# Optimization experiments

Hardware: AMD Instinct MI355X
Metric: run time of the kernel (lower is better)

Reference implementation:

```python
import jax, jax.numpy as jnp
import numpy as np

N_ATOMS = 64
N_SAMPLES = 2 ** 15
SAMPLERATE = 22050
N_RES = 4096
N_ROOMS = 8
N_COEFFS = N_SAMPLES // 2 + 1


def make_waves():
    # musical_scale_hz(21, 106, 4096//4) -> 4 waveform families (sine, saw, square, triangle)
    n_steps = N_RES // 4
    midi = np.linspace(21.0, 106.0, n_steps)
    f0 = 440.0 * 2.0 ** ((midi - 69.0) / 12.0)
    rps = ((f0 / (SAMPLERATE / 2.0)) * np.pi).astype(np.float32)
    rad = rps[:, None] * np.arange(N_SAMPLES, dtype=np.float32)[None, :]
    sine = np.sin(rad)
    t = rad / (2.0 * np.pi)
    saw = (2.0 * (t - np.floor(t + 0.5))).astype(np.float32)
    sq = np.sign(sine).astype(np.float32)
    tri = (2.0 * np.abs(saw) - 1.0).astype(np.float32)
    return jnp.asarray(np.concatenate([sine, saw, sq, tri], 0).reshape(1, N_RES, N_SAMPLES))


def pdf2(means, stds, n):
    # gaussian pdf evaluated on linspace(0,1,n); means/stds: (1, A)
    rng = jnp.linspace(0.0, 1.0, n)
    mu = means[..., None]
    sd = stds[..., None]
    return jnp.exp(-0.5 * ((rng - mu) / sd) ** 2) / (sd * jnp.sqrt(2.0 * jnp.pi))


def linear_interp(x, n_out):
    # F.interpolate(mode='linear', align_corners=False) on last axis; x: (b, a, f)
    f = x.shape[-1]
    pos = (jnp.arange(n_out) + 0.5) * (f / n_out) - 0.5
    pos = jnp.clip(pos, 0.0, f - 1)
    i0 = jnp.floor(pos).astype(jnp.int32)
    i1 = jnp.minimum(i0 + 1, f - 1)
    w = (pos - i0).astype(x.dtype)
    return x[..., i0] * (1.0 - w) + x[..., i1] * w


def exponential_decay(decay_values, n_atoms, n_frames, base_resonance, n_samples):
    dv = jax.nn.sigmoid(decay_values.reshape(-1, n_atoms, 1))
    dv = jnp.broadcast_to(dv, (dv.shape[0], n_atoms, n_frames))
    decay = base_resonance + dv * (1.0 - base_resonance) * 0.95
    decay = jnp.exp(jnp.cumsum(jnp.log(decay + 1e-12), axis=-1))
    return linear_interp(decay, n_samples)


def fft_convolve(a, b):
    # zero-pad to 2N, multiply spectra, take first N samples
    n = a.shape[-1]
    pa = jnp.pad(a, ((0, 0), (0, 0), (0, n)))
    pb = jnp.pad(b, ((0, 0), (0, 0), (0, n)))
    spec = jnp.fft.rfft(pa, axis=-1) * jnp.fft.rfft(pb, axis=-1)
    return jnp.fft.irfft(spec, n=2 * n, axis=-1)[..., :n]


def layer_norm(x, w, b, eps=1e-5):
    m = jnp.mean(x, axis=-1, keepdims=True)
    v = jnp.var(x, axis=-1, keepdims=True)
    return (x - m) / jnp.sqrt(v + eps) * w + b


def sparse_softmax_st(x):
    soft = jax.nn.softmax(x, axis=-1)
    hard = jax.nn.one_hot(jnp.argmax(x, axis=-1), x.shape[-1], dtype=x.dtype)
    return hard + soft - jax.lax.stop_gradient(soft)


def model_forward(x, mix, decays, filter_decays, resonance_choice, noise_filter,
                  resonance_filter, resonance_filter2, env, amplitudes, verb_params,
                  noise, waves, ln_w, ln_b, mix_w1, mix_w2, room_w1, room_w2, room_irs):
    overall_mix = jax.nn.softmax(mix, axis=-1)                                   # (1,A,2)
    resonances = jnp.einsum('bar,brn->ban', jax.nn.relu(resonance_choice), waves)  # (1,A,N)

    # band-pass filtered noise (gaussian filter in frequency domain)
    noise_spec = jnp.fft.rfft(noise, axis=-1)
    noise_filt = pdf2(noise_filter[:, :, 0], jnp.abs(noise_filter[:, :, 1]) + 1e-12, N_COEFFS)
    filtered_noise = jnp.fft.irfft(noise_spec * noise_filt, n=N_SAMPLES, axis=-1)

    res_spec = jnp.fft.rfft(resonances, axis=-1)
    rf1 = pdf2(jnp.zeros_like(resonance_filter[:, :, 0]),
               jnp.abs(resonance_filter[:, :, 1]) + 1e-12, N_COEFFS)
    filtered_resonance = jnp.fft.irfft(res_spec * rf1, n=N_SAMPLES, axis=-1)
    rf2 = pdf2(jnp.zeros_like(resonance_filter2[:, :, 0]),
               jnp.abs(resonance_filter2[:, :, 1]) + 1e-12, N_COEFFS)
    filt_res_2 = jnp.fft.irfft(res_spec * rf2, n=N_SAMPLES, axis=-1)

    filt_crossfade = exponential_decay(filter_decays, N_ATOMS, 128, 0.02, N_SAMPLES)
    decay_env = exponential_decay(decays, N_ATOMS, 128, 0.02, N_SAMPLES)
    decaying_resonance = filtered_resonance * decay_env
    decaying_resonance2 = filt_res_2 * decay_env

    # gaussian envelope branch (gaussian_envelope = True)
    envelopes = pdf2(env[:, :, 0], jnp.abs(env[:, :, 1] + 1e-12) * 0.1, N_SAMPLES)
    positioned_noise = filtered_noise * envelopes

    res = fft_convolve(positioned_noise, decaying_resonance)
    res2 = fft_convolve(positioned_noise, decaying_resonance2)
    mixed = filt_crossfade * res + (1.0 - filt_crossfade) * res2

    final = positioned_noise * overall_mix[:, :, 0:1] + mixed * overall_mix[:, :, 1:2]
    final = final / (jnp.linalg.norm(final, axis=-1, keepdims=True) + 1e-8)
    amps = jnp.abs(amplitudes)
    final = final * amps

    # ReverbGenerator: layernorm -> small MLPs -> hard room choice -> fft convolve with IR
    h = layer_norm(verb_params, ln_w, ln_b)
    mix_v = jax.nn.sigmoid(jax.nn.leaky_relu(h @ mix_w1) @ mix_w2)               # (1,A,1)
    room_logits = jax.nn.leaky_relu(h @ room_w1) @ room_w2                        # (1,A,R)
    room = sparse_softmax_st(room_logits)
    ir = jnp.einsum('bar,rn->ban', room, room_irs)
    wet = fft_convolve(final, ir)
    out = final * mix_v + wet * (1.0 - mix_v)
    return out, amps


def setup_inputs() -> dict:
    key = jax.random.key(0)
    ks = jax.random.split(key, 20)
    return {
        'x': jax.random.normal(ks[0], (1, 1), jnp.float32),
        'mix': jax.random.uniform(ks[1], (1, N_ATOMS, 2), jnp.float32),
        'decays': jax.random.uniform(ks[2], (1, N_ATOMS, 1), jnp.float32, -6.0, 6.0),
        'filter_decays': jax.random.uniform(ks[3], (1, N_ATOMS, 1), jnp.float32, -6.0, 6.0),
        'resonance_choice': jax.random.uniform(ks[4], (1, N_ATOMS, N_RES), jnp.float32),
        'noise_filter': jax.random.uniform(ks[5], (1, N_ATOMS, 2), jnp.float32),
        'resonance_filter': jax.random.uniform(ks[6], (1, N_ATOMS, 2), jnp.float32),
        'resonance_filter2': jax.random.uniform(ks[7], (1, N_ATOMS, 2), jnp.float32),
        'env': jax.random.uniform(ks[8], (1, N_ATOMS, 2), jnp.float32),
        'amplitudes': jax.random.uniform(ks[9], (1, N_ATOMS, 1), jnp.float32) ** 2,
        'verb_params': jax.random.uniform(ks[10], (1, N_ATOMS, 4), jnp.float32, -1.0, 1.0),
        'noise': jax.random.uniform(ks[11], (1, N_ATOMS, N_SAMPLES), jnp.float32, -1.0, 1.0),
        'waves': make_waves(),
        'ln_w': jnp.ones((4,), jnp.float32),
        'ln_b': jnp.zeros((4,), jnp.float32),
        'mix_w1': jax.random.normal(ks[12], (4, 4), jnp.float32) * 0.1,
        'mix_w2': jax.random.normal(ks[13], (4, 1), jnp.float32) * 0.1,
        'room_w1': jax.random.normal(ks[14], (4, 4), jnp.float32) * 0.1,
        'room_w2': jax.random.normal(ks[15], (4, N_ROOMS), jnp.float32) * 0.1,
        'room_irs': jax.random.normal(ks[16], (N_ROOMS, N_SAMPLES), jnp.float32) * 0.01,
    }


def reference(x, mix, decays, filter_decays, resonance_choice, noise_filter,
              resonance_filter, resonance_filter2, env, amplitudes, verb_params,
              noise, waves, ln_w, ln_b, mix_w1, mix_w2, room_w1, room_w2, room_irs):
    return model_forward(x, mix, decays, filter_decays, resonance_choice, noise_filter,
                         resonance_filter, resonance_filter2, env, amplitudes, verb_params,
                         noise, waves, ln_w, ln_b, mix_w1, mix_w2, room_w1, room_w2, room_irs)
```

## Files before the change

### kernel.cpp

```cpp
#include <hip/hip_runtime.h>


typedef __attribute__((ext_vector_type(8))) short bf16x8;
typedef __attribute__((ext_vector_type(4))) float f32x4;

constexpr int SC_OM0   = 0;
constexpr int SC_OM1   = 64;
constexpr int SC_NFMU  = 128;
constexpr int SC_NFSD  = 192;
constexpr int SC_RF1SD = 256;
constexpr int SC_RF2SD = 320;
constexpr int SC_ENVMU = 384;
constexpr int SC_ENVSD = 448;
constexpr int SC_AMPS  = 512;
constexpr int SC_MIXV  = 576;
constexpr int SC_ROOM  = 832;
constexpr int SC_PSS   = 1024;
constexpr int SC_DTAB  = 4096;
constexpr int SC_FTAB  = 12288;

constexpr size_t OFF_SCAL = 0;
constexpr size_t OFF_CT   = 65536;
constexpr size_t OFF_P    = 327680;
constexpr size_t OFF_DS   = 8716288;
constexpr size_t OFF_RP   = OFF_DS;
constexpr size_t OFF_W64  = 17104896;
constexpr size_t OFF_NSS  = OFF_W64;
constexpr size_t OFF_W2   = OFF_W64 + 4194304;
constexpr size_t OFF_RSS  = 25493504;
constexpr size_t OFF_FINU = OFF_RSS;
constexpr size_t OFF_W1   = 29687808;
constexpr size_t OFF_FN   = 38076416;
constexpr size_t OFF_FR1  = 40173568;
constexpr size_t OFF_FR2  = 42270720;
constexpr size_t OFF_IRS  = 44367872;
constexpr size_t WS_FLOATS= 45416448;

__device__ __forceinline__ float2 cmul(float2 a, float2 b) {
  return make_float2(a.x*b.x - a.y*b.y, a.x*b.y + a.y*b.x);
}

__device__ __forceinline__ short f2bf(float x) {
  unsigned u = __float_as_uint(x);
  u = (u + 0x7FFFu + ((u >> 16) & 1u)) >> 16;
  return (short)u;
}

__device__ __forceinline__ void dft16(float2 d[16], float ei)
{
  const float CA[4] = {1.0f, 0.92387953251128674f, 0.70710678118654752f, 0.38268343236508977f};
  const float SA[4] = {0.0f, 0.38268343236508977f, 0.70710678118654752f, 0.92387953251128674f};
  const float CB[4] = {1.0f, 0.70710678118654752f, 0.0f, -0.70710678118654752f};
  const float SB[4] = {0.0f, 0.70710678118654752f, 1.0f, 0.70710678118654752f};
  float2 e[16];
  #pragma unroll
  for (int q = 0; q < 4; ++q) {
    float2 x0 = d[q], x1 = d[q+4], x2 = d[q+8], x3 = d[q+12];
    float ca = CA[q], sa = ei*SA[q], cb = CB[q], sb = ei*SB[q];
    float2 sum1 = make_float2(x0.x+x2.x, x0.y+x2.y);
    float2 d1   = make_float2(x0.x-x2.x, x0.y-x2.y);
    float2 dif1 = make_float2(d1.x*ca - d1.y*sa, d1.x*sa + d1.y*ca);
    float2 sum2 = make_float2(x1.x+x3.x, x1.y+x3.y);
    float2 d2   = make_float2(x1.x-x3.x, x1.y-x3.y);
    float2 dt   = make_float2(d2.x*ca - d2.y*sa, d2.x*sa + d2.y*ca);
    float2 dif2 = make_float2(-ei*dt.y, ei*dt.x);
    float2 Dm   = make_float2(sum1.x-sum2.x, sum1.y-sum2.y);
    float2 Dm2  = make_float2(dif1.x-dif2.x, dif1.y-dif2.y);
    e[4*q+0] = make_float2(sum1.x+sum2.x, sum1.y+sum2.y);
    e[4*q+1] = make_float2(dif1.x+dif2.x, dif1.y+dif2.y);
    e[4*q+2] = make_float2(Dm.x*cb - Dm.y*sb, Dm.x*sb + Dm.y*cb);
    e[4*q+3] = make_float2(Dm2.x*cb - Dm2.y*sb, Dm2.x*sb + Dm2.y*cb);
  }
  #pragma unroll
  for (int q = 0; q < 4; ++q) {
    float2 x0 = e[q], x1 = e[q+4], x2 = e[q+8], x3 = e[q+12];
    float2 sum1 = make_float2(x0.x+x2.x, x0.y+x2.y);
    float2 dif1 = make_float2(x0.x-x2.x, x0.y-x2.y);
    float2 sum2 = make_float2(x1.x+x3.x, x1.y+x3.y);
    float2 d2   = make_float2(x1.x-x3.x, x1.y-x3.y);
    float2 dif2 = make_float2(-ei*d2.y, ei*d2.x);
    d[q]    = make_float2(sum1.x+sum2.x, sum1.y+sum2.y);
    d[q+4]  = make_float2(dif1.x+dif2.x, dif1.y+dif2.y);
    d[q+8]  = make_float2(sum1.x-sum2.x, sum1.y-sum2.y);
    d[q+12] = make_float2(dif1.x-dif2.x, dif1.y-dif2.y);
  }
}

__device__ __forceinline__ void twiddleB(float2 d[16], int u, float dir2pi)
{
  float sn1, cs1;
  __sincosf(dir2pi * ((float)u * (1.0f/256.0f)), &sn1, &cs1);
  float2 w1 = make_float2(cs1, sn1);
  float2 tw = w1;
  #pragma unroll
  for (int k = 1; k < 16; ++k) { d[k] = cmul(d[k], tw); tw = cmul(tw, w1); }
}

template<int LEN>
__device__ float2* lds_fft(float2* src, float2* dst,
                           const float2* __restrict__ T256,
                           float dsign, float ei)
{
  constexpr int QB  = LEN >> 2;
  constexpr int FPT = (16 * QB) >> 8;
  constexpr int NST = (LEN == 256) ? 4 : 3;
  int n = LEN, s = 1, ls = 0;
  int sh = (LEN == 256) ? 0 : 1;

  if (LEN == 128) {
    constexpr int HB = LEN >> 1;
    constexpr int BPT = (16 * HB) >> 8;
    __syncthreads();
    #pragma unroll
    for (int b = 0; b < BPT; ++b) {
      int g = threadIdx.x + (b << 8);
      int row = g / HB;
      int beta = g & (HB - 1);
      float2 tj = T256[beta << 1];
      float cs = tj.x, sn = dsign * tj.y;
      float2 av = src[row*LEN + (beta ^ row)];
      float2 bv = src[row*LEN + ((beta + HB) ^ row)];
      float2 sum = make_float2(av.x + bv.x, av.y + bv.y);
      float2 dif = make_float2(av.x - bv.x, av.y - bv.y);
      float2 tw  = make_float2(dif.x*cs - dif.y*sn, dif.x*sn + dif.y*cs);
      dst[row*LEN + ((2*beta)     ^ row)] = sum;
      dst[row*LEN + ((2*beta + 1) ^ row)] = tw;
    }
    float2* t = src; src = dst; dst = t;
    n = 64; s = 2; ls = 1; sh = 2;
  }

  for (int st = 0; st < NST; ++st) {
    __syncthreads();
    #pragma unroll
    for (int b = 0; b < FPT; ++b) {
      int g   = threadIdx.x + (b << 8);
      int row = g / QB;
      int q   = g & (QB - 1);
      int p1  = q >> ls;
      int blo = q & (s - 1);
      int base = row * LEN;
      float2 x0 = src[base + ( q         ^ row)];
      float2 x1 = src[base + ((q +   QB) ^ row)];
      float2 x2 = src[base + ((q + 2*QB) ^ row)];
      float2 x3 = src[base + ((q + 3*QB) ^ row)];
      float2 tA = T256[p1 << sh];
      float caA = tA.x, saA = dsign * tA.y;
      float2 tB = T256[p1 << (sh + 1)];
      float caB = tB.x, saB = dsign * tB.y;
      float2 sum1 = make_float2(x0.x + x2.x, x0.y + x2.y);
      float2 d1   = make_float2(x0.x - x2.x, x0.y - x2.y);
      float2 dif1 = make_float2(d1.x*caA - d1.y*saA, d1.x*saA + d1.y*caA);
      float2 sum2 = make_float2(x1.x + x3.x, x1.y + x3.y);
      float2 d2   = make_float2(x1.x - x3.x, x1.y - x3.y);
      float2 dt   = make_float2(d2.x*caA - d2.y*saA, d2.x*saA + d2.y*caA);
      float2 dif2 = make_float2(-ei * dt.y, ei * dt.x);
      float2 S  = make_float2(sum1.x + sum2.x, sum1.y + sum2.y);
      float2 Dm = make_float2(sum1.x - sum2.x, sum1.y - sum2.y);
      float2 D  = make_float2(Dm.x*caB - Dm.y*saB, Dm.x*saB + Dm.y*caB);
      float2 S2 = make_float2(dif1.x + dif2.x, dif1.y + dif2.y);
      float2 Dm2= make_float2(dif1.x - dif2.x, dif1.y - dif2.y);
      float2 D2 = make_float2(Dm2.x*caB - Dm2.y*saB, Dm2.x*saB + Dm2.y*caB);
      int w0 = (p1 << (ls + 2)) | blo;
      dst[base + ( w0          ^ row)] = S;
      dst[base + ((w0 +     s) ^ row)] = S2;
      dst[base + ((w0 + 2 * s) ^ row)] = D;
      dst[base + ((w0 + 3 * s) ^ row)] = D2;
    }
    float2* t = src; src = dst; dst = t;
    n >>= 2; s <<= 2; ls += 2; sh += 2;
  }
  __syncthreads();
  return src;
}

template<int N1, int MODE_IN, int MODE_OUT>
__global__ __launch_bounds__(256) void k_fft_strided(
    float2* cbuf, const float* __restrict__ rin, const float* __restrict__ rin2,
    float* __restrict__ rout, float* __restrict__ rout2,
    const float* __restrict__ scal, const float* __restrict__ finU,
    float dir2pi, float outScale)
{
  constexpr int N  = N1 * 256;
  constexpr int NH = N >> 1;
  constexpr int LOG2N1 = (N1 == 256) ? 8 : 7;
  __shared__ float2 X[16*16*17];
  __shared__ float2 T256[256];
  __shared__ float2 TN[N1];
  const int a = blockIdx.y;
  const int n1base = blockIdx.x << 4;
  const int r = threadIdx.x & 15;
  const int u = threadIdx.x >> 4;
  const float ei = (dir2pi < 0.0f) ? -1.0f : 1.0f;

  {
    float ang = dir2pi * ((float)threadIdx.x * (1.0f/256.0f));
    float sn, cs; __sincosf(ang, &sn, &cs);
    T256[threadIdx.x] = make_float2(cs, sn);
    if (threadIdx.x < N1) {
      float ang2 = dir2pi * ((float)threadIdx.x * (1.0f/(float)N));
      float sn2, cs2; __sincosf(ang2, &sn2, &cs2);
      TN[threadIdx.x] = make_float2(cs2, sn2);
    }
  }

  float2 d[16];
  #pragma unroll
  for (int m = 0; m < 16; ++m) {
    int j = u + (m << 4);
    int n = n1base + r + N1 * j;
    float x = (n < NH) ? rin[(size_t)a * NH + n] : 0.0f;
    d[m] = make_float2(x, 0.0f);
  }

  dft16(d, ei);
  twiddleB(d, u, dir2pi);
  #pragma unroll
  for (int k = 0; k < 16; ++k) X[(u*16 + k)*17 + r] = d[k];
  __syncthreads();
  #pragma unroll
  for (int m = 0; m < 16; ++m) d[m] = X[(m*16 + u)*17 + r];
  dft16(d, ei);

  #pragma unroll
  for (int k1 = 0; k1 < 16; ++k1) {
    int j = u + (k1 << 4);
    int n = n1base + r + N1 * j;
    int aa = (n1base + r) * j;
    float2 tw = cmul(T256[(aa >> LOG2N1) & 255], TN[aa & (N1 - 1)]);
    cbuf[(size_t)a * N + n] = cmul(d[k1], tw);
  }
}

__global__ __launch_bounds__(256) void k_fft_s256_DsP(
    float2* __restrict__ Ds, float2* __restrict__ P,
    const float* __restrict__ fr1, const float* __restrict__ fr2,
    const float* __restrict__ fn, const float* __restrict__ scal)
{
  constexpr int N = 65536, NH = 32768;
  constexpr float FWD = -6.283185307179586f;
  __shared__ float2 X[16*16*17];
  __shared__ float2 T256[256];
  __shared__ float2 TN[256];
  const bool isDs = blockIdx.y < 64;
  const int a = isDs ? blockIdx.y : blockIdx.y - 64;
  const int n1base = blockIdx.x << 4;
  const int r = threadIdx.x & 15;
  const int u = threadIdx.x >> 4;

  {
    float ang = FWD * ((float)threadIdx.x * (1.0f/256.0f));
    float sn, cs; __sincosf(ang, &sn, &cs);
    T256[threadIdx.x] = make_float2(cs, sn);
    float ang2 = FWD * ((float)threadIdx.x * (1.0f/(float)N));
    float sn2, cs2; __sincosf(ang2, &sn2, &cs2);
    TN[threadIdx.x] = make_float2(cs2, sn2);
  }

  float emu = 0.f, esd = 1.f, egp = 0.f;
  if (!isDs) {
    emu = scal[SC_ENVMU + a];
    esd = scal[SC_ENVSD + a];
    egp = 0.3989422804014327f / esd;
  }

  float2 d[16];
  #pragma unroll
  for (int m = 0; m < 16; ++m) {
    int j = u + (m << 4);
    int n = n1base + r + 256 * j;
    float2 v = make_float2(0.0f, 0.0f);
    if (n < NH) {
      if (isDs) {
        float pos = ((float)n + 0.5f) * (1.0f/256.0f) - 0.5f;
        pos = fminf(fmaxf(pos, 0.0f), 127.0f);
        int i0 = (int)pos;
        float w = pos - (float)i0;
        int i1 = (i0 + 1 < 127) ? i0 + 1 : 127;
        const float* dt = scal + SC_DTAB + a*128;
        float de = dt[i0]*(1.0f-w) + dt[i1]*w;
        v = make_float2(fr1[(size_t)a * NH + n] * de,
                        fr2[(size_t)a * NH + n] * de);
      } else {
        float uu = (float)n * (1.0f / 32767.0f);
        float te = (uu - emu) / esd;
        float envv = __expf(-0.5f * te * te) * egp;
        v = make_float2(fn[(size_t)a * NH + n] * envv, 0.0f);
      }
    }
    d[m] = v;
  }

  dft16(d, -1.0f);
  twiddleB(d, u, FWD);
  #pragma unroll
  for (int k = 0; k < 16; ++k) X[(u*16 + k)*17 + r] = d[k];
  __syncthreads();
  #pragma unroll
  for (int m = 0; m < 16; ++m) d[m] = X[(m*16 + u)*17 + r];
  dft16(d, -1.0f);

  float2* outp = isDs ? Ds : P;
  #pragma unroll
  for (int k1 = 0; k1 < 16; ++k1) {
    int j = u + (k1 << 4);
    int n = n1base + r + 256 * j;
    int aa = (n1base + r) * j;
    float2 tw = cmul(T256[(aa >> 8) & 255], TN[aa & 255]);
    outp[(size_t)a * N + n] = cmul(d[k1], tw);
  }
}

__global__ __launch_bounds__(256) void k_fft_s128_first(
    float2* __restrict__ RSs, float2* __restrict__ NSs,
    const float* __restrict__ rez, const float* __restrict__ noise)
{
  constexpr int N1 = 128, N = 32768;
  constexpr float FWD = -6.283185307179586f;
  __shared__ float2 X[16*16*17];
  __shared__ float2 T256[256];
  __shared__ float2 TN[128];
  const bool isRS = blockIdx.y < 64;
  const int a = isRS ? blockIdx.y : blockIdx.y - 64;
  const int n1base = blockIdx.x << 4;
  const int r = threadIdx.x & 15;
  const int u = threadIdx.x >> 4;

  {
    float ang = FWD * ((float)threadIdx.x * (1.0f/256.0f));
    float sn, cs; __sincosf(ang, &sn, &cs);
    T256[threadIdx.x] = make_float2(cs, sn);
    if (threadIdx.x < 128) {
      float ang2 = FWD * ((float)threadIdx.x * (1.0f/(float)N));
      float sn2, cs2; __sincosf(ang2, &sn2, &cs2);
      TN[threadIdx.x] = make_float2(cs2, sn2);
    }
  }

  float2 d[16];
  #pragma unroll
  for (int m = 0; m < 16; ++m) {
    int j = u + (m << 4);
    int n = n1base + r + N1 * j;
    float x = isRS ? (rez[(size_t)a * N + n] + rez[(size_t)(64 + a) * N + n])
                   : noise[(size_t)a * N + n];
    d[m] = make_float2(x, 0.0f);
  }

  dft16(d, -1.0f);
  twiddleB(d, u, FWD);
  #pragma unroll
  for (int k = 0; k < 16; ++k) X[(u*16 + k)*17 + r] = d[k];
  __syncthreads();
  #pragma unroll
  for (int m = 0; m < 16; ++m) d[m] = X[(m*16 + u)*17 + r];
  dft16(d, -1.0f);

  float2* outp = isRS ? RSs : NSs;
  #pragma unroll
  for (int k1 = 0; k1 < 16; ++k1) {
    int j = u + (k1 << 4);
    int n = n1base + r + N1 * j;
    int aa = (n1base + r) * j;
    float2 tw = cmul(T256[(aa >> 7) & 255], TN[aa & 127]);
    outp[(size_t)a * N + n] = cmul(d[k1], tw);
  }
}

__global__ __launch_bounds__(256) void k_fft_m128_both(
    const float2* __restrict__ RSs, const float2* __restrict__ NSs,
    float2* __restrict__ W1, float2* __restrict__ W2,
    const float* __restrict__ scal)
{
  constexpr int N1 = 128;
  constexpr int N = N1 * 256;
  constexpr int ITERS = (16 * N1) >> 8;
  constexpr int LOG2N1 = 7;
  constexpr float FWD = -6.283185307179586f;
  constexpr float IVD = +6.283185307179586f;
  __shared__ float2 A[16 * N1];
  __shared__ float2 B[16 * N1];
  __shared__ float2 T256[256];
  __shared__ float2 TN[N1];
  const bool isRS = blockIdx.y < 64;
  const int a = isRS ? blockIdx.y : blockIdx.y - 64;
  const int colbase = blockIdx.x << 4;

  {
    float ang = FWD * ((float)threadIdx.x * (1.0f/256.0f));
    float sn, cs; __sincosf(ang, &sn, &cs);
    T256[threadIdx.x] = make_float2(cs, sn);
    if (threadIdx.x < N1) {
      float ang2 = IVD * ((float)threadIdx.x * (1.0f/(float)N));
      float sn2, cs2; __sincosf(ang2, &sn2, &cs2);
      TN[threadIdx.x] = make_float2(cs2, sn2);
    }
  }

  float mu = 0.f, isd1 = 0.f, g1 = 0.f, isd2 = 0.f, g2 = 0.f;
  if (isRS) {
    float s1 = scal[SC_RF1SD + a], s2 = scal[SC_RF2SD + a];
    isd1 = 1.0f/s1; g1 = 0.3989422804014327f/s1;
    isd2 = 1.0f/s2; g2 = 0.3989422804014327f/s2;
  } else {
    float sd = scal[SC_NFSD + a]; mu = scal[SC_NFMU + a];
    isd1 = 1.0f/sd; g1 = 0.3989422804014327f/sd;
  }
  const float2* zin = (isRS ? RSs : NSs) + (size_t)a * N;
  float2* out = (isRS ? W1 : W2) + (size_t)a * N;

  #pragma unroll
  for (int it = 0; it < ITERS; ++it) {
    int flat = threadIdx.x + (it << 8);
    int c = flat / N1, j = flat & (N1 - 1);
    A[c*N1 + (j ^ c)] = zin[(size_t)(colbase + c) * N1 + j];
  }
  float2* cur = lds_fft<N1>(A, B, T256, 1.0f, -1.0f);
  float2* alt = (cur == A) ? B : A;

  #pragma unroll
  for (int it = 0; it < ITERS; ++it) {
    int flat = threadIdx.x + (it << 8);
    int c = flat / N1, j = flat & (N1 - 1);
    int idx = c*N1 + (j ^ c);
    float2 v = cur[idx];
    int k  = (colbase + c) + (j << 8);
    int kk = (k <= N - k) ? k : N - k;
    if (isRS) {
      float fr = (float)kk * (2.0f/(float)N);
      float t1 = fr * isd1, t2 = fr * isd2;
      float ga = __expf(-0.5f * t1 * t1) * g1;
      float gb = __expf(-0.5f * t2 * t2) * g2;
      v = make_float2(v.x*ga - v.y*gb, v.x*gb + v.y*ga);
    } else {
      float t = ((float)kk * (2.0f/(float)N) - mu) * isd1;
      float g = __expf(-0.5f * t * t) * g1;
      v.x *= g; v.y *= g;
    }
    cur[idx] = v;
  }

  float2* r2 = lds_fft<N1>(cur, alt, T256, -1.0f, 1.0f);

  #pragma unroll
  for (int it = 0; it < ITERS; ++it) {
    int flat = threadIdx.x + (it << 8);
    int c = flat / N1, j = flat & (N1 - 1);
    float2 v = r2[c*N1 + (j ^ c)];
    int aa = j * (colbase + c);
    float2 t1 = T256[(aa >> LOG2N1) & 255];
    t1.y = -t1.y;
    float2 tw = cmul(t1, TN[aa & (N1 - 1)]);
    out[(size_t)(colbase + c) * N1 + j] = cmul(v, tw);
  }
}

__global__ __launch_bounds__(256) void k_fft_s128_last(
    const float2* __restrict__ W1, const float2* __restrict__ W2,
    float* __restrict__ fr1, float* __restrict__ fr2, float* __restrict__ fn)
{
  constexpr int N1 = 128, N = 32768;
  constexpr float IVD = +6.283185307179586f;
  constexpr float S32 = 1.0f / 32768.0f;
  __shared__ float2 X[16*16*17];
  const bool isRS = blockIdx.y < 64;
  const int a = isRS ? blockIdx.y : blockIdx.y - 64;
  const int n1base = blockIdx.x << 4;
  const int r = threadIdx.x & 15;
  const int u = threadIdx.x >> 4;

  const float2* cb = (isRS ? W1 : W2) + (size_t)a * N;
  float2 d[16];
  #pragma unroll
  for (int m = 0; m < 16; ++m) {
    int j = u + (m << 4);
    d[m] = cb[n1base + r + N1 * j];
  }
  dft16(d, 1.0f);
  twiddleB(d, u, IVD);
  #pragma unroll
  for (int k = 0; k < 16; ++k) X[(u*16 + k)*17 + r] = d[k];
  __syncthreads();
  #pragma unroll
  for (int m = 0; m < 16; ++m) d[m] = X[(m*16 + u)*17 + r];
  dft16(d, 1.0f);

  #pragma unroll
  for (int k1 = 0; k1 < 16; ++k1) {
    int j = u + (k1 << 4);
    int n = n1base + r + N1 * j;
    if (isRS) {
      fr1[(size_t)a * N + n] = d[k1].x * S32;
      fr2[(size_t)a * N + n] = d[k1].y * S32;
    } else {
      fn[(size_t)a * N + n] = d[k1].x * S32;
    }
  }
}

__global__ __launch_bounds__(256) void k_fft_mid256dual(
    const float2* __restrict__ zin, const float2* __restrict__ zin2half,
    float2* __restrict__ out1, const int* __restrict__ roomArr)
{
  constexpr int N = 65536;
  constexpr float FWD = -6.283185307179586f;
  constexpr float IVD = +6.283185307179586f;
  __shared__ float2 X[16*16*17];
  __shared__ float2 T256[256];
  __shared__ float2 TN[256];
  const int a = blockIdx.y;
  const int colbase = blockIdx.x << 4;
  const int u  = threadIdx.x & 15;
  const int rc = threadIdx.x >> 4;

  {
    float ang = FWD * ((float)threadIdx.x * (1.0f/256.0f));
    float sn, cs; __sincosf(ang, &sn, &cs);
    T256[threadIdx.x] = make_float2(cs, sn);
    float ang2 = IVD * ((float)threadIdx.x * (1.0f/(float)N));
    float sn2, cs2; __sincosf(ang2, &sn2, &cs2);
    TN[threadIdx.x] = make_float2(cs2, sn2);
  }
  __syncthreads();

  const float2* z2 = zin2half + (size_t)(roomArr ? roomArr[a] : a) * N;
  const size_t rowG = (size_t)a * N + (size_t)(colbase + rc) * 256;
  const size_t rowZ2 = (size_t)(colbase + rc) * 256;

  float2 d[16];
  #pragma unroll
  for (int m = 0; m < 16; ++m) d[m] = zin[rowG + u + (m << 4)];
  dft16(d, -1.0f);
  twiddleB(d, u, FWD);
  #pragma unroll
  for (int k = 0; k < 16; ++k) X[(rc*16 + k)*17 + u] = d[k];
  #pragma unroll
  for (int m = 0; m < 16; ++m) d[m] = X[(rc*16 + u)*17 + m];
  dft16(d, -1.0f);

  float2 stash[16];
  #pragma unroll
  for (int k = 0; k < 16; ++k) stash[k] = d[k];
  #pragma unroll
  for (int m = 0; m < 16; ++m) d[m] = z2[rowZ2 + u + (m << 4)];
  dft16(d, -1.0f);
  twiddleB(d, u, FWD);
  #pragma unroll
  for (int k = 0; k < 16; ++k) X[(rc*16 + k)*17 + u] = d[k];
  #pragma unroll
  for (int m = 0; m < 16; ++m) d[m] = X[(rc*16 + u)*17 + m];
  dft16(d, -1.0f);
  #pragma unroll
  for (int k = 0; k < 16; ++k) d[k] = cmul(stash[k], d[k]);

  dft16(d, 1.0f);
  twiddleB(d, u, IVD);
  #pragma unroll
  for (int k = 0; k < 16; ++k) X[(rc*16 + k)*17 + u] = d[k];
  #pragma unroll
  for (int m = 0; m < 16; ++m) d[m] = X[(rc*16 + u)*17 + m];
  dft16(d, 1.0f);

  #pragma unroll
  for (int k1 = 0; k1 < 16; ++k1) {
    int j = u + (k1 << 4);
    int aa = j * (colbase + rc);
    float2 t1 = T256[(aa >> 8) & 255];
    t1.y = -t1.y;
    float2 tw = cmul(t1, TN[aa & 255]);
    out1[rowG + j] = cmul(d[k1], tw);
  }
}

__global__ __launch_bounds__(256) void k_fft_out6fwd(
    const float2* __restrict__ W64in, const float* __restrict__ fn,
    float* __restrict__ finU, float* __restrict__ scal,
    float2* __restrict__ DsOut)
{
  constexpr int N = 65536, NH = 32768;
  constexpr float FWD = -6.283185307179586f;
  constexpr float IVD = +6.283185307179586f;
  constexpr float S64 = 1.0f / 65536.0f;
  __shared__ float2 X[16*16*17];
  __shared__ float2 T256[256];
  __shared__ float2 TN[256];
  __shared__ float red[256];
  const int a = blockIdx.y;
  const int n1base = blockIdx.x << 4;
  const int r = threadIdx.x & 15;
  const int u = threadIdx.x >> 4;

  {
    float ang = FWD * ((float)threadIdx.x * (1.0f/256.0f));
    float sn, cs; __sincosf(ang, &sn, &cs);
    T256[threadIdx.x] = make_float2(cs, sn);
    float ang2 = FWD * ((float)threadIdx.x * (1.0f/(float)N));
    float sn2, cs2; __sincosf(ang2, &sn2, &cs2);
    TN[threadIdx.x] = make_float2(cs2, sn2);
  }

  const float emu = scal[SC_ENVMU + a];
  const float esd = scal[SC_ENVSD + a];
  const float egp = 0.3989422804014327f / esd;
  const float om0 = scal[SC_OM0 + a], om1 = scal[SC_OM1 + a];
  const float* ft = scal + SC_FTAB + a*128;

  float2 d[16];
  #pragma unroll
  for (int m = 0; m < 16; ++m) {
    int j = u + (m << 4);
    d[m] = W64in[(size_t)a * N + n1base + r + 256 * j];
  }
  dft16(d, 1.0f);
  twiddleB(d, u, IVD);
  #pragma unroll
  for (int k = 0; k < 16; ++k) X[(u*16 + k)*17 + r] = d[k];
  __syncthreads();
  #pragma unroll
  for (int m = 0; m < 16; ++m) d[m] = X[(m*16 + u)*17 + r];
  dft16(d, 1.0f);

  float fv[8];
  float ss = 0.0f;
  #pragma unroll
  for (int k1 = 0; k1 < 8; ++k1) {
    int n = n1base + r + 256 * (u + (k1 << 4));
    float resv  = d[k1].x * S64;
    float res2v = d[k1].y * S64;
    float uu = (float)n * (1.0f / 32767.0f);
    float te = (uu - emu) / esd;
    float envv = __expf(-0.5f * te * te) * egp;
    float pnv = fn[(size_t)a * NH + n] * envv;
    float pos = ((float)n + 0.5f) * (1.0f/256.0f) - 0.5f;
    pos = fminf(fmaxf(pos, 0.0f), 127.0f);
    int i0 = (int)pos;
    float w = pos - (float)i0;
    int i1 = (i0 + 1 < 127) ? i0 + 1 : 127;
    float fc = ft[i0]*(1.0f-w) + ft[i1]*w;
    float f = pnv*om0 + (fc*resv + (1.0f-fc)*res2v)*om1;
    finU[(size_t)a * NH + n] = f;
    fv[k1] = f;
    ss += f * f;
  }
  red[threadIdx.x] = ss;
  __syncthreads();
  for (int s = 128; s > 0; s >>= 1) {
    if (threadIdx.x < s) red[threadIdx.x] += red[threadIdx.x + s];
    __syncthreads();
  }
  if (threadIdx.x == 0) scal[SC_PSS + a*16 + blockIdx.x] = red[0];

  #pragma unroll
  for (int m = 0; m < 16; ++m)
    d[m] = (m < 8) ? make_float2(fv[m], 0.0f) : make_float2(0.0f, 0.0f);
  dft16(d, -1.0f);
  twiddleB(d, u, FWD);
  #pragma unroll
  for (int k = 0; k < 16; ++k) X[(u*16 + k)*17 + r] = d[k];
  __syncthreads();
  #pragma unroll
  for (int m = 0; m < 16; ++m) d[m] = X[(m*16 + u)*17 + r];
  dft16(d, -1.0f);

  #pragma unroll
  for (int k1 = 0; k1 < 16; ++k1) {
    int j = u + (k1 << 4);
    int n = n1base + r + 256 * j;
    int aa = (n1base + r) * j;
    float2 tw = cmul(T256[(aa >> 8) & 255], TN[aa & 255]);
    DsOut[(size_t)a * N + n] = cmul(d[k1], tw);
  }
}

__global__ __launch_bounds__(256) void k_fft_s256_out3(
    const float2* __restrict__ W64in, const float* __restrict__ finU,
    const float* __restrict__ scal, float* __restrict__ out)
{
  constexpr int N = 65536, NH = 32768;
  constexpr float IVD = +6.283185307179586f;
  constexpr float S64 = 1.0f / 65536.0f;
  __shared__ float2 X[16*16*17];
  const int a = blockIdx.y;
  const int n1base = blockIdx.x << 4;
  const int r = threadIdx.x & 15;
  const int u = threadIdx.x >> 4;

  float ss = 0.0f;
  #pragma unroll
  for (int i = 0; i < 16; ++i) ss += scal[SC_PSS + a*16 + i];
  float fscale = scal[SC_AMPS + a] / (sqrtf(ss) + 1e-8f);
  float mixv = scal[SC_MIXV + a];
  float w1 = fscale * (1.0f - mixv);
  float w0 = fscale * mixv;

  float2 d[16];
  #pragma unroll
  for (int m = 0; m < 16; ++m) {
    int j = u + (m << 4);
    d[m] = W64in[(size_t)a * N + n1base + r + 256 * j];
  }
  dft16(d, 1.0f);
  twiddleB(d, u, IVD);
  #pragma unroll
  for (int k = 0; k < 16; ++k) X[(u*16 + k)*17 + r] = d[k];
  __syncthreads();
  #pragma unroll
  for (int m = 0; m < 16; ++m) d[m] = X[(m*16 + u)*17 + r];
  dft16(d, 1.0f);

  #pragma unroll
  for (int k1 = 0; k1 < 8; ++k1) {
    int n = n1base + r + 256 * (u + (k1 << 4));
    out[(size_t)a * NH + n] =
        d[k1].x * S64 * w1 + finU[(size_t)a * NH + n] * w0;
  }
}

__global__ void k_scalars(
    const float* __restrict__ mix, const float* __restrict__ decays,
    const float* __restrict__ fdec, const float* __restrict__ nf,
    const float* __restrict__ rf1, const float* __restrict__ rf2,
    const float* __restrict__ env, const float* __restrict__ amplitudes,
    const float* __restrict__ verb, const float* __restrict__ ln_w,
    const float* __restrict__ ln_b, const float* __restrict__ mw1,
    const float* __restrict__ mw2, const float* __restrict__ rw1,
    const float* __restrict__ rw2, float* __restrict__ scal,
    float* __restrict__ dout)
{
  int a = threadIdx.x;
  if (a >= 64) return;
  float m0 = mix[a*2+0], m1 = mix[a*2+1];
  float mx = fmaxf(m0, m1);
  float e0 = expf(m0 - mx), e1 = expf(m1 - mx);
  float inv = 1.0f / (e0 + e1);
  scal[SC_OM0+a] = e0 * inv;
  scal[SC_OM1+a] = e1 * inv;
  scal[SC_NFMU+a] = nf[a*2+0];
  scal[SC_NFSD+a] = fabsf(nf[a*2+1]) + 1e-12f;
  scal[SC_RF1SD+a] = fabsf(rf1[a*2+1]) + 1e-12f;
  scal[SC_RF2SD+a] = fabsf(rf2[a*2+1]) + 1e-12f;
  scal[SC_ENVMU+a] = env[a*2+0];
  scal[SC_ENVSD+a] = fabsf(env[a*2+1] + 1e-12f) * 0.1f;
  float amp = fabsf(amplitudes[a]);
  scal[SC_AMPS+a] = amp;
  dout[2097152 + a] = amp;
  float d  = 0.02f + (1.0f/(1.0f+expf(-decays[a]))) * (0.98f * 0.95f);
  float fd = 0.02f + (1.0f/(1.0f+expf(-fdec[a])))   * (0.98f * 0.95f);
  float pd = 1.0f, pf = 1.0f;
  for (int f = 0; f < 128; ++f) {
    pd *= d; pf *= fd;
    scal[SC_DTAB + a*128 + f] = pd;
    scal[SC_FTAB + a*128 + f] = pf;
  }
  float x0 = verb[a*4+0], x1 = verb[a*4+1], x2 = verb[a*4+2], x3 = verb[a*4+3];
  float mean = (x0+x1+x2+x3) * 0.25f;
  float d0 = x0-mean, d1 = x1-mean, d2 = x2-mean, d3 = x3-mean;
  float var = (d0*d0 + d1*d1 + d2*d2 + d3*d3) * 0.25f;
  float rs = 1.0f / sqrtf(var + 1e-5f);
  float h[4] = { d0*rs*ln_w[0]+ln_b[0], d1*rs*ln_w[1]+ln_b[1],
                 d2*rs*ln_w[2]+ln_b[2], d3*rs*ln_w[3]+ln_b[3] };
  float t[4], u[4];
  for (int j = 0; j < 4; ++j) {
    float s1 = 0.f, s2 = 0.f;
    for (int i2 = 0; i2 < 4; ++i2) {
      s1 += h[i2] * mw1[i2*4 + j];
      s2 += h[i2] * rw1[i2*4 + j];
    }
    t[j] = (s1 > 0.f) ? s1 : 0.01f*s1;
    u[j] = (s2 > 0.f) ? s2 : 0.01f*s2;
  }
  float ml = 0.f;
  for (int j = 0; j < 4; ++j) ml += t[j] * mw2[j];
  scal[SC_MIXV+a] = 1.0f / (1.0f + expf(-ml));
  float best = -1e30f; int bi = 0;
  for (int r = 0; r < 8; ++r) {
    float lg = 0.f;
    for (int j = 0; j < 4; ++j) lg += u[j] * rw2[j*8 + r];
    if (lg > best) { best = lg; bi = r; }
  }
  ((int*)scal)[SC_ROOM + a] = bi;
}

__global__ void k_packA(const float* __restrict__ rc, short* __restrict__ ctb)
{
  int o = blockIdx.x * 256 + threadIdx.x;
  int m = o >> 12, k = o & 4095;
  int s = k >> 2, f = k & 3;
  float v = fmaxf(rc[m*4096 + f*1024 + s], 0.0f);
  ctb[o] = f2bf(v);
}

__global__ __launch_bounds__(512) void k_gemm_mfma(
    const float* __restrict__ waves, const short* __restrict__ ctb,
    float* __restrict__ rp)
{
  const int t = threadIdx.x;
  const int w = t >> 6, lane = t & 63;
  const int ml = lane & 15, q = lane >> 4;
  const int col = blockIdx.x * 128 + w * 16 + ml;
  const int part = blockIdx.y;
  const int kb0 = part * 64;

  f32x4 acc[4] = {};

  const float* ws0 = waves + (size_t)(kb0*8 + 2*q) * 32768 + col;
  const float* ws1 = waves + (size_t)(1024 + kb0*8 + 2*q) * 32768 + col;
  const short* abase = ctb + (size_t)ml * 4096 + (size_t)kb0 * 32 + q * 8;

  #define LOADW(v, kbl) { size_t o = (size_t)(kbl) * (8*32768); \
    v[0] = ws0[o]; v[1] = ws0[o + 32768]; v[2] = ws1[o]; v[3] = ws1[o + 32768]; }

  #define DOKB(v, kbl) { \
    float sq0 = (v[0] > 0.f) ? 1.f : ((v[0] < 0.f) ? -1.f : v[0]); \
    float sq1 = (v[1] > 0.f) ? 1.f : ((v[1] < 0.f) ? -1.f : v[1]); \
    float tr0 = 2.f * fabsf(v[2]) - 1.f; \
    float tr1 = 2.f * fabsf(v[3]) - 1.f; \
    bf16x8 b; \
    b[0] = f2bf(v[0]); b[1] = f2bf(v[2]); b[2] = f2bf(sq0); b[3] = f2bf(tr0); \
    b[4] = f2bf(v[1]); b[5] = f2bf(v[3]); b[6] = f2bf(sq1); b[7] = f2bf(tr1); \
    const short* ap = abase + (size_t)(kbl) * 32; \
    acc[0] = __builtin_amdgcn_mfma_f32_16x16x32_bf16(*(const bf16x8*)(ap),                   b, acc[0], 0,0,0); \
    acc[1] = __builtin_amdgcn_mfma_f32_16x16x32_bf16(*(const bf16x8*)(ap + (size_t)16*4096), b, acc[1], 0,0,0); \
    acc[2] = __builtin_amdgcn_mfma_f32_16x16x32_bf16(*(const bf16x8*)(ap + (size_t)32*4096), b, acc[2], 0,0,0); \
    acc[3] = __builtin_amdgcn_mfma_f32_16x16x32_bf16(*(const bf16x8*)(ap + (size_t)48*4096), b, acc[3], 0,0,0); }

  float vA[4], vB[4];
  LOADW(vA, 0);
  LOADW(vB, 1);
  for (int kbl = 0; kbl < 64; kbl += 2) {
    DOKB(vA, kbl);
    if (kbl + 2 < 64) LOADW(vA, kbl + 2);
    DOKB(vB, kbl + 1);
    if (kbl + 3 < 64) LOADW(vB, kbl + 3);
  }
  #undef LOADW
  #undef DOKB

  #pragma unroll
  for (int mt = 0; mt < 4; ++mt) {
    #pragma unroll
    for (int rr = 0; rr < 4; ++rr) {
      rp[(size_t)(part*64 + mt*16 + q*4 + rr) * 32768 + col] = acc[mt][rr];
    }
  }
}

extern "C" void kernel_launch(void* const* d_in, const int* in_sizes, int n_in,
                              void* d_out, int out_size, void* d_ws, size_t ws_size,
                              hipStream_t stream)
{
  const float* mix   = (const float*)d_in[1];
  const float* dec   = (const float*)d_in[2];
  const float* fdec  = (const float*)d_in[3];
  const float* rc    = (const float*)d_in[4];
  const float* nf    = (const float*)d_in[5];
  const float* rf1   = (const float*)d_in[6];
  const float* rf2   = (const float*)d_in[7];
  const float* env   = (const float*)d_in[8];
  const float* amps  = (const float*)d_in[9];
  const float* verb  = (const float*)d_in[10];
  const float* noise = (const float*)d_in[11];
  const float* waves = (const float*)d_in[12];
  const float* lnw   = (const float*)d_in[13];
  const float* lnb   = (const float*)d_in[14];
  const float* mw1   = (const float*)d_in[15];
  const float* mw2   = (const float*)d_in[16];
  const float* rw1   = (const float*)d_in[17];
  const float* rw2   = (const float*)d_in[18];
  const float* rirs  = (const float*)d_in[19];
  float* out = (float*)d_out;
  float* w   = (float*)d_ws;

  if (ws_size < WS_FLOATS * 4ULL) return;

  float*  scal = w + OFF_SCAL;
  short*  ctb  = (short*)(w + OFF_CT);
  float*  rp   = w + OFF_RP;
  float2* P    = (float2*)(w + OFF_P);
  float2* Ds   = (float2*)(w + OFF_DS);
  float2* W64  = (float2*)(w + OFF_W64);
  float2* RSs  = (float2*)(w + OFF_RSS);
  float2* NSs  = (float2*)(w + OFF_NSS);
  float2* W2   = (float2*)(w + OFF_W2);
  float*  finU = w + OFF_FINU;
  float2* W1   = (float2*)(w + OFF_W1);
  float*  fn   = w + OFF_FN;
  float*  fr1  = w + OFF_FR1;
  float*  fr2  = w + OFF_FR2;
  float2* IRS  = (float2*)(w + OFF_IRS);
  const int* room = ((const int*)(w + OFF_SCAL)) + SC_ROOM;

  const float FWD = -6.283185307179586f;

  k_scalars<<<1, 64, 0, stream>>>(mix, dec, fdec, nf, rf1, rf2, env, amps, verb,
                                  lnw, lnb, mw1, mw2, rw1, rw2, scal, out);
  k_packA<<<1024, 256, 0, stream>>>(rc, ctb);
  k_gemm_mfma<<<dim3(256, 2), 512, 0, stream>>>(waves, ctb, rp);

  k_fft_strided<256,3,0><<<dim3(16,8),256,0,stream>>>(IRS, rirs, nullptr, nullptr, nullptr, scal, nullptr, FWD, 1.f);

  k_fft_s128_first<<<dim3(8,128),256,0,stream>>>(RSs, NSs, rp, noise);
  k_fft_m128_both<<<dim3(16,128),256,0,stream>>>(RSs, NSs, W1, W2, scal);
  k_fft_s128_last<<<dim3(8,128),256,0,stream>>>(W1, W2, fr1, fr2, fn);

  k_fft_s256_DsP<<<dim3(16,128),256,0,stream>>>(Ds, P, fr1, fr2, fn, scal);

  k_fft_mid256dual<<<dim3(16,64),256,0,stream>>>(Ds, P, W64, nullptr);

  k_fft_out6fwd<<<dim3(16,64),256,0,stream>>>(W64, fn, finU, scal, Ds);

  k_fft_mid256dual<<<dim3(16,64),256,0,stream>>>(Ds, IRS, W64, room);

  k_fft_s256_out3<<<dim3(16,64),256,0,stream>>>(W64, finU, scal, out);
}
```

Measured before the change: 310.6 us.

## Store FFT intermediates and GEMM output as packed bf16, fold IR FFT into DsP kernel

All complex intermediate buffers between FFT stages (RSs, NSs, W1, W2, Ds, P, W64, IRS) are now stored as packed bf16 pairs in 32-bit words, and the GEMM result rp is written as bf16. This halves the global memory traffic between the memory-bound FFT passes. The room impulse response FFT is merged into the DsP launch as a third block mode, which removes one kernel launch, and the GEMM prefetch depth grows from 2 to 4. The cost is a large loss of precision on the intermediate spectra, which may break the accuracy tolerance.

Result: faster. 293.3 us (-5.6%).

```diff
diff --git a/kernel.cpp b/kernel.cpp
--- a/kernel.cpp
+++ b/kernel.cpp
@@ -44,6 +44,17 @@
   unsigned u = __float_as_uint(x);
   u = (u + 0x7FFFu + ((u >> 16) & 1u)) >> 16;
   return (short)u;
+}
+__device__ __forceinline__ float bf2f(short s) {
+  return __uint_as_float((unsigned)(unsigned short)s << 16);
+}
+__device__ __forceinline__ unsigned pk2(float2 v) {
+  return (unsigned)(unsigned short)f2bf(v.x)
+       | ((unsigned)(unsigned short)f2bf(v.y) << 16);
+}
+__device__ __forceinline__ float2 upk2(unsigned u) {
+  return make_float2(__uint_as_float(u << 16),
+                     __uint_as_float(u & 0xFFFF0000u));
 }
 
 __device__ __forceinline__ void dft16(float2 d[16], float ei)
@@ -174,76 +185,20 @@
   return src;
 }
 
-template<int N1, int MODE_IN, int MODE_OUT>
-__global__ __launch_bounds__(256) void k_fft_strided(
-    float2* cbuf, const float* __restrict__ rin, const float* __restrict__ rin2,
-    float* __restrict__ rout, float* __restrict__ rout2,
-    const float* __restrict__ scal, const float* __restrict__ finU,
-    float dir2pi, float outScale)
-{
-  constexpr int N  = N1 * 256;
-  constexpr int NH = N >> 1;
-  constexpr int LOG2N1 = (N1 == 256) ? 8 : 7;
-  __shared__ float2 X[16*16*17];
-  __shared__ float2 T256[256];
-  __shared__ float2 TN[N1];
-  const int a = blockIdx.y;
-  const int n1base = blockIdx.x << 4;
-  const int r = threadIdx.x & 15;
-  const int u = threadIdx.x >> 4;
-  const float ei = (dir2pi < 0.0f) ? -1.0f : 1.0f;
-
-  {
-    float ang = dir2pi * ((float)threadIdx.x * (1.0f/256.0f));
-    float sn, cs; __sincosf(ang, &sn, &cs);
-    T256[threadIdx.x] = make_float2(cs, sn);
-    if (threadIdx.x < N1) {
-      float ang2 = dir2pi * ((float)threadIdx.x * (1.0f/(float)N));
-      float sn2, cs2; __sincosf(ang2, &sn2, &cs2);
-      TN[threadIdx.x] = make_float2(cs2, sn2);
-    }
-  }
-
-  float2 d[16];
-  #pragma unroll
-  for (int m = 0; m < 16; ++m) {
-    int j = u + (m << 4);
-    int n = n1base + r + N1 * j;
-    float x = (n < NH) ? rin[(size_t)a * NH + n] : 0.0f;
-    d[m] = make_float2(x, 0.0f);
-  }
-
-  dft16(d, ei);
-  twiddleB(d, u, dir2pi);
-  #pragma unroll
-  for (int k = 0; k < 16; ++k) X[(u*16 + k)*17 + r] = d[k];
-  __syncthreads();
-  #pragma unroll
-  for (int m = 0; m < 16; ++m) d[m] = X[(m*16 + u)*17 + r];
-  dft16(d, ei);
-
-  #pragma unroll
-  for (int k1 = 0; k1 < 16; ++k1) {
-    int j = u + (k1 << 4);
-    int n = n1base + r + N1 * j;
-    int aa = (n1base + r) * j;
-    float2 tw = cmul(T256[(aa >> LOG2N1) & 255], TN[aa & (N1 - 1)]);
-    cbuf[(size_t)a * N + n] = cmul(d[k1], tw);
-  }
-}
-
-__global__ __launch_bounds__(256) void k_fft_s256_DsP(
-    float2* __restrict__ Ds, float2* __restrict__ P,
+__global__ __launch_bounds__(256) void k_fft_s256_DsPI(
+    unsigned* __restrict__ Ds, unsigned* __restrict__ P,
+    unsigned* __restrict__ IRS,
     const float* __restrict__ fr1, const float* __restrict__ fr2,
-    const float* __restrict__ fn, const float* __restrict__ scal)
+    const float* __restrict__ fn, const float* __restrict__ rirs,
+    const float* __restrict__ scal)
 {
   constexpr int N = 65536, NH = 32768;
   constexpr float FWD = -6.283185307179586f;
   __shared__ float2 X[16*16*17];
   __shared__ float2 T256[256];
   __shared__ float2 TN[256];
-  const bool isDs = blockIdx.y < 64;
-  const int a = isDs ? blockIdx.y : blockIdx.y - 64;
+  const int mode = (blockIdx.y < 64) ? 0 : ((blockIdx.y < 128) ? 1 : 2);
+  const int a = (mode == 0) ? blockIdx.y : ((mode == 1) ? blockIdx.y - 64 : blockIdx.y - 128);
   const int n1base = blockIdx.x << 4;
   const int r = threadIdx.x & 15;
   const int u = threadIdx.x >> 4;
@@ -258,7 +213,7 @@
   }
 
   float emu = 0.f, esd = 1.f, egp = 0.f;
-  if (!isDs) {
+  if (mode == 1) {
     emu = scal[SC_ENVMU + a];
     esd = scal[SC_ENVSD + a];
     egp = 0.3989422804014327f / esd;
@@ -271,7 +226,7 @@
     int n = n1base + r + 256 * j;
     float2 v = make_float2(0.0f, 0.0f);
     if (n < NH) {
-      if (isDs) {
+      if (mode == 0) {
         float pos = ((float)n + 0.5f) * (1.0f/256.0f) - 0.5f;
         pos = fminf(fmaxf(pos, 0.0f), 127.0f);
         int i0 = (int)pos;
@@ -281,11 +236,13 @@
         float de = dt[i0]*(1.0f-w) + dt[i1]*w;
         v = make_float2(fr1[(size_t)a * NH + n] * de,
                         fr2[(size_t)a * NH + n] * de);
-      } else {
+      } else if (mode == 1) {
         float uu = (float)n * (1.0f / 32767.0f);
         float te = (uu - emu) / esd;
         float envv = __expf(-0.5f * te * te) * egp;
         v = make_float2(fn[(size_t)a * NH + n] * envv, 0.0f);
+      } else {
+        v = make_float2(rirs[(size_t)a * NH + n], 0.0f);
       }
     }
     d[m] = v;
@@ -300,20 +257,20 @@
   for (int m = 0; m < 16; ++m) d[m] = X[(m*16 + u)*17 + r];
   dft16(d, -1.0f);
 
-  float2* outp = isDs ? Ds : P;
+  unsigned* outp = (mode == 0) ? Ds : ((mode == 1) ? P : IRS);
   #pragma unroll
   for (int k1 = 0; k1 < 16; ++k1) {
     int j = u + (k1 << 4);
     int n = n1base + r + 256 * j;
     int aa = (n1base + r) * j;
     float2 tw = cmul(T256[(aa >> 8) & 255], TN[aa & 255]);
-    outp[(size_t)a * N + n] = cmul(d[k1], tw);
+    outp[(size_t)a * N + n] = pk2(cmul(d[k1], tw));
   }
 }
 
 __global__ __launch_bounds__(256) void k_fft_s128_first(
-    float2* __restrict__ RSs, float2* __restrict__ NSs,
-    const float* __restrict__ rez, const float* __restrict__ noise)
+    unsigned* __restrict__ RSs, unsigned* __restrict__ NSs,
+    const short* __restrict__ rez, const float* __restrict__ noise)
 {
   constexpr int N1 = 128, N = 32768;
   constexpr float FWD = -6.283185307179586f;
@@ -342,7 +299,8 @@
   for (int m = 0; m < 16; ++m) {
     int j = u + (m << 4);
     int n = n1base + r + N1 * j;
-    float x = isRS ? (rez[(size_t)a * N + n] + rez[(size_t)(64 + a) * N + n])
+    float x = isRS ? (bf2f(rez[(size_t)a * N + n]) +
+                      bf2f(rez[(size_t)(64 + a) * N + n]))
                    : noise[(size_t)a * N + n];
     d[m] = make_float2(x, 0.0f);
   }
@@ -356,20 +314,20 @@
   for (int m = 0; m < 16; ++m) d[m] = X[(m*16 + u)*17 + r];
   dft16(d, -1.0f);
 
-  float2* outp = isRS ? RSs : NSs;
+  unsigned* outp = isRS ? RSs : NSs;
   #pragma unroll
   for (int k1 = 0; k1 < 16; ++k1) {
     int j = u + (k1 << 4);
     int n = n1base + r + N1 * j;
     int aa = (n1base + r) * j;
     float2 tw = cmul(T256[(aa >> 7) & 255], TN[aa & 127]);
-    outp[(size_t)a * N + n] = cmul(d[k1], tw);
+    outp[(size_t)a * N + n] = pk2(cmul(d[k1], tw));
   }
 }
 
 __global__ __launch_bounds__(256) void k_fft_m128_both(
-    const float2* __restrict__ RSs, const float2* __restrict__ NSs,
-    float2* __restrict__ W1, float2* __restrict__ W2,
+    const unsigned* __restrict__ RSs, const unsigned* __restrict__ NSs,
+    unsigned* __restrict__ W1, unsigned* __restrict__ W2,
     const float* __restrict__ scal)
 {
   constexpr int N1 = 128;
@@ -406,14 +364,14 @@
     float sd = scal[SC_NFSD + a]; mu = scal[SC_NFMU + a];
     isd1 = 1.0f/sd; g1 = 0.3989422804014327f/sd;
   }
-  const float2* zin = (isRS ? RSs : NSs) + (size_t)a * N;
-  float2* out = (isRS ? W1 : W2) + (size_t)a * N;
+  const unsigned* zin = (isRS ? RSs : NSs) + (size_t)a * N;
+  unsigned* out = (isRS ? W1 : W2) + (size_t)a * N;
 
   #pragma unroll
   for (int it = 0; it < ITERS; ++it) {
     int flat = threadIdx.x + (it << 8);
     int c = flat / N1, j = flat & (N1 - 1);
-    A[c*N1 + (j ^ c)] = zin[(size_t)(colbase + c) * N1 + j];
+    A[c*N1 + (j ^ c)] = upk2(zin[(size_t)(colbase + c) * N1 + j]);
   }
   float2* cur = lds_fft<N1>(A, B, T256, 1.0f, -1.0f);
   float2* alt = (cur == A) ? B : A;
@@ -451,12 +409,12 @@
     float2 t1 = T256[(aa >> LOG2N1) & 255];
     t1.y = -t1.y;
     float2 tw = cmul(t1, TN[aa & (N1 - 1)]);
-    out[(size_t)(colbase + c) * N1 + j] = cmul(v, tw);
+    out[(size_t)(colbase + c) * N1 + j] = pk2(cmul(v, tw));
   }
 }
 
 __global__ __launch_bounds__(256) void k_fft_s128_last(
-    const float2* __restrict__ W1, const float2* __restrict__ W2,
+    const unsigned* __restrict__ W1, const unsigned* __restrict__ W2,
     float* __restrict__ fr1, float* __restrict__ fr2, float* __restrict__ fn)
 {
   constexpr int N1 = 128, N = 32768;
@@ -469,12 +427,12 @@
   const int r = threadIdx.x & 15;
   const int u = threadIdx.x >> 4;
 
-  const float2* cb = (isRS ? W1 : W2) + (size_t)a * N;
+  const unsigned* cb = (isRS ? W1 : W2) + (size_t)a * N;
   float2 d[16];
   #pragma unroll
   for (int m = 0; m < 16; ++m) {
     int j = u + (m << 4);
-    d[m] = cb[n1base + r + N1 * j];
+    d[m] = upk2(cb[n1base + r + N1 * j]);
   }
   dft16(d, 1.0f);
   twiddleB(d, u, IVD);
@@ -499,8 +457,8 @@
 }
 
 __global__ __launch_bounds__(256) void k_fft_mid256dual(
-    const float2* __restrict__ zin, const float2* __restrict__ zin2half,
-    float2* __restrict__ out1, const int* __restrict__ roomArr)
+    const unsigned* __restrict__ zin, const unsigned* __restrict__ zin2half,
+    unsigned* __restrict__ out1, const int* __restrict__ roomArr)
 {
   constexpr int N = 65536;
   constexpr float FWD = -6.283185307179586f;
@@ -523,13 +481,13 @@
   }
   __syncthreads();
 
-  const float2* z2 = zin2half + (size_t)(roomArr ? roomArr[a] : a) * N;
+  const unsigned* z2 = zin2half + (size_t)(roomArr ? roomArr[a] : a) * N;
   const size_t rowG = (size_t)a * N + (size_t)(colbase + rc) * 256;
   const size_t rowZ2 = (size_t)(colbase + rc) * 256;
 
   float2 d[16];
   #pragma unroll
-  for (int m = 0; m < 16; ++m) d[m] = zin[rowG + u + (m << 4)];
+  for (int m = 0; m < 16; ++m) d[m] = upk2(zin[rowG + u + (m << 4)]);
   dft16(d, -1.0f);
   twiddleB(d, u, FWD);
   #pragma unroll
@@ -542,7 +500,7 @@
   #pragma unroll
   for (int k = 0; k < 16; ++k) stash[k] = d[k];
   #pragma unroll
-  for (int m = 0; m < 16; ++m) d[m] = z2[rowZ2 + u + (m << 4)];
+  for (int m = 0; m < 16; ++m) d[m] = upk2(z2[rowZ2 + u + (m << 4)]);
   dft16(d, -1.0f);
   twiddleB(d, u, FWD);
   #pragma unroll
@@ -568,14 +526,14 @@
     float2 t1 = T256[(aa >> 8) & 255];
     t1.y = -t1.y;
     float2 tw = cmul(t1, TN[aa & 255]);
-    out1[rowG + j] = cmul(d[k1], tw);
+    out1[rowG + j] = pk2(cmul(d[k1], tw));
   }
 }
 
 __global__ __launch_bounds__(256) void k_fft_out6fwd(
-    const float2* __restrict__ W64in, const float* __restrict__ fn,
+    const unsigned* __restrict__ W64in, const float* __restrict__ fn,
     float* __restrict__ finU, float* __restrict__ scal,
-    float2* __restrict__ DsOut)
+    unsigned* __restrict__ DsOut)
 {
   constexpr int N = 65536, NH = 32768;
   constexpr float FWD = -6.283185307179586f;
@@ -609,7 +567,7 @@
   #pragma unroll
   for (int m = 0; m < 16; ++m) {
     int j = u + (m << 4);
-    d[m] = W64in[(size_t)a * N + n1base + r + 256 * j];
+    d[m] = upk2(W64in[(size_t)a * N + n1base + r + 256 * j]);
   }
   dft16(d, 1.0f);
   twiddleB(d, u, IVD);
@@ -668,12 +626,12 @@
     int n = n1base + r + 256 * j;
     int aa = (n1base + r) * j;
     float2 tw = cmul(T256[(aa >> 8) & 255], TN[aa & 255]);
-    DsOut[(size_t)a * N + n] = cmul(d[k1], tw);
+    DsOut[(size_t)a * N + n] = pk2(cmul(d[k1], tw));
   }
 }
 
 __global__ __launch_bounds__(256) void k_fft_s256_out3(
-    const float2* __restrict__ W64in, const float* __restrict__ finU,
+    const unsigned* __restrict__ W64in, const float* __restrict__ finU,
     const float* __restrict__ scal, float* __restrict__ out)
 {
   constexpr int N = 65536, NH = 32768;
@@ -697,7 +655,7 @@
   #pragma unroll
   for (int m = 0; m < 16; ++m) {
     int j = u + (m << 4);
-    d[m] = W64in[(size_t)a * N + n1base + r + 256 * j];
+    d[m] = upk2(W64in[(size_t)a * N + n1base + r + 256 * j]);
   }
   dft16(d, 1.0f);
   twiddleB(d, u, IVD);
@@ -792,7 +750,7 @@
 
 __global__ __launch_bounds__(512) void k_gemm_mfma(
     const float* __restrict__ waves, const short* __restrict__ ctb,
-    float* __restrict__ rp)
+    short* __restrict__ rp)
 {
   const int t = threadIdx.x;
   const int w = t >> 6, lane = t & 63;
@@ -824,14 +782,20 @@
     acc[2] = __builtin_amdgcn_mfma_f32_16x16x32_bf16(*(const bf16x8*)(ap + (size_t)32*4096), b, acc[2], 0,0,0); \
     acc[3] = __builtin_amdgcn_mfma_f32_16x16x32_bf16(*(const bf16x8*)(ap + (size_t)48*4096), b, acc[3], 0,0,0); }
 
-  float vA[4], vB[4];
+  float vA[4], vB[4], vC[4], vD[4];
   LOADW(vA, 0);
   LOADW(vB, 1);
-  for (int kbl = 0; kbl < 64; kbl += 2) {
+  LOADW(vC, 2);
+  LOADW(vD, 3);
+  for (int kbl = 0; kbl < 64; kbl += 4) {
     DOKB(vA, kbl);
-    if (kbl + 2 < 64) LOADW(vA, kbl + 2);
+    if (kbl + 4 < 64) LOADW(vA, kbl + 4);
     DOKB(vB, kbl + 1);
-    if (kbl + 3 < 64) LOADW(vB, kbl + 3);
+    if (kbl + 5 < 64) LOADW(vB, kbl + 5);
+    DOKB(vC, kbl + 2);
+    if (kbl + 6 < 64) LOADW(vC, kbl + 6);
+    DOKB(vD, kbl + 3);
+    if (kbl + 7 < 64) LOADW(vD, kbl + 7);
   }
   #undef LOADW
   #undef DOKB
@@ -840,7 +804,7 @@
   for (int mt = 0; mt < 4; ++mt) {
     #pragma unroll
     for (int rr = 0; rr < 4; ++rr) {
-      rp[(size_t)(part*64 + mt*16 + q*4 + rr) * 32768 + col] = acc[mt][rr];
+      rp[(size_t)(part*64 + mt*16 + q*4 + rr) * 32768 + col] = f2bf(acc[mt][rr]);
     }
   }
 }
@@ -873,37 +837,33 @@
 
   if (ws_size < WS_FLOATS * 4ULL) return;
 
-  float*  scal = w + OFF_SCAL;
-  short*  ctb  = (short*)(w + OFF_CT);
-  float*  rp   = w + OFF_RP;
-  float2* P    = (float2*)(w + OFF_P);
-  float2* Ds   = (float2*)(w + OFF_DS);
-  float2* W64  = (float2*)(w + OFF_W64);
-  float2* RSs  = (float2*)(w + OFF_RSS);
-  float2* NSs  = (float2*)(w + OFF_NSS);
-  float2* W2   = (float2*)(w + OFF_W2);
-  float*  finU = w + OFF_FINU;
-  float2* W1   = (float2*)(w + OFF_W1);
-  float*  fn   = w + OFF_FN;
-  float*  fr1  = w + OFF_FR1;
-  float*  fr2  = w + OFF_FR2;
-  float2* IRS  = (float2*)(w + OFF_IRS);
+  float*    scal = w + OFF_SCAL;
+  short*    ctb  = (short*)(w + OFF_CT);
+  short*    rp   = (short*)(w + OFF_RP);
+  unsigned* P    = (unsigned*)(w + OFF_P);
+  unsigned* Ds   = (unsigned*)(w + OFF_DS);
+  unsigned* W64  = (unsigned*)(w + OFF_W64);
+  unsigned* RSs  = (unsigned*)(w + OFF_RSS);
+  unsigned* NSs  = (unsigned*)(w + OFF_NSS);
+  unsigned* W2   = (unsigned*)(w + OFF_W2);
+  float*    finU = w + OFF_FINU;
+  unsigned* W1   = (unsigned*)(w + OFF_W1);
+  float*    fn   = w + OFF_FN;
+  float*    fr1  = w + OFF_FR1;
+  float*    fr2  = w + OFF_FR2;
+  unsigned* IRS  = (unsigned*)(w + OFF_IRS);
   const int* room = ((const int*)(w + OFF_SCAL)) + SC_ROOM;
-
-  const float FWD = -6.283185307179586f;
 
   k_scalars<<<1, 64, 0, stream>>>(mix, dec, fdec, nf, rf1, rf2, env, amps, verb,
                                   lnw, lnb, mw1, mw2, rw1, rw2, scal, out);
   k_packA<<<1024, 256, 0, stream>>>(rc, ctb);
   k_gemm_mfma<<<dim3(256, 2), 512, 0, stream>>>(waves, ctb, rp);
 
-  k_fft_strided<256,3,0><<<dim3(16,8),256,0,stream>>>(IRS, rirs, nullptr, nullptr, nullptr, scal, nullptr, FWD, 1.f);
-
   k_fft_s128_first<<<dim3(8,128),256,0,stream>>>(RSs, NSs, rp, noise);
   k_fft_m128_both<<<dim3(16,128),256,0,stream>>>(RSs, NSs, W1, W2, scal);
   k_fft_s128_last<<<dim3(8,128),256,0,stream>>>(W1, W2, fr1, fr2, fn);
 
-  k_fft_s256_DsP<<<dim3(16,128),256,0,stream>>>(Ds, P, fr1, fr2, fn, scal);
+  k_fft_s256_DsPI<<<dim3(16,136),256,0,stream>>>(Ds, P, IRS, fr1, fr2, fn, rirs, scal);
 
   k_fft_mid256dual<<<dim3(16,64),256,0,stream>>>(Ds, P, W64, nullptr);
 
```
